# Kernel tuning notes

Measured on AMD Instinct MI355X. Metric: run time of the kernel, lower is better.

Reference implementation:

```python
import jax, jax.numpy as jnp
import numpy as np

B, H, S, D = 4, 16, 2048, 64

def setup_inputs() -> dict:
    key = jax.random.key(0)
    k1, k2, k3 = jax.random.split(key, 3)
    x1 = jax.random.normal(k1, (B, H, S, D), dtype=jnp.float32)
    x2 = jax.random.normal(k2, (B, H, S, D), dtype=jnp.float32)
    x3 = jax.random.normal(k3, (B, H, S, D), dtype=jnp.float32)
    scale = jnp.float32(1.0 / np.sqrt(D))  # 0.125
    return {"x1": x1, "x2": x2, "x3": x3, "scale": scale}

def reference(x1, x2, x3, scale):
    # scores: [B, H, S, S] = Q @ K^T * scale
    scores = jnp.einsum('bhqd,bhkd->bhqk', x1, x2) * scale
    att = jax.nn.softmax(scores, axis=-1)
    # out: [B, H, S, D] = att @ V
    return jnp.einsum('bhqk,bhkd->bhqd', att, x3)
```

## Files before the change

kernel.cpp:

```cpp
#include <hip/hip_runtime.h>
#include <hip/hip_bf16.h>

typedef __attribute__((ext_vector_type(8))) short short8;
typedef __attribute__((ext_vector_type(16))) float f32x16;
typedef __attribute__((ext_vector_type(2))) unsigned uint2v;
typedef unsigned long long ull;

#define S_LEN 2048
#define D_DIM 64
#define QT 256
#define KT 64
#define NT (S_LEN / KT)
#define SMAXC 16.0f
#define SWZ(r) ((((r) & 7) ^ (((r) >> 3) & 7)) << 4)

static __device__ __forceinline__ unsigned cvt_pk(float lo, float hi) {
  unsigned r;
  asm("v_cvt_pk_bf16_f32 %0, %1, %2" : "=v"(r) : "v"(lo), "v"(hi));
  return r;
}

static __device__ __forceinline__ void plswap(unsigned &a, unsigned &b) {
  uint2v r = __builtin_amdgcn_permlane32_swap(a, b, false, false);
  a = r.x; b = r.y;
}

union U8 { unsigned u[4]; short8 s; };

__global__ __attribute__((amdgpu_flat_work_group_size(256, 256),
                          amdgpu_waves_per_eu(2, 2)))
void attn_fwd(const float* __restrict__ Qg, const float* __restrict__ Kg,
              const float* __restrict__ Vg, const float* __restrict__ sp,
              float* __restrict__ Og)
{
  __shared__ __align__(16) char smem[32768];

  const int tid = threadIdx.x;
  const int w   = tid >> 6;
  const int l   = tid & 63;
  const int q32 = l & 31;
  const int hi  = l >> 5;

  const int wg   = blockIdx.x;
  const int xcd  = wg & 7;
  const int slot = wg >> 3;
  const int bh   = xcd * 8 + (slot >> 3);
  const int qb   = (slot & 7) * QT;

  const float* Qh = Qg + (size_t)bh * (S_LEN * D_DIM);
  const float* Kh = Kg + (size_t)bh * (S_LEN * D_DIM);
  const float* Vh = Vg + (size_t)bh * (S_LEN * D_DIM);
  float*       Oh = Og + (size_t)bh * (S_LEN * D_DIM);

  const float qscale = sp[0] * 1.4426950408889634f;

  short8 qfa[4], qfb[4];
#pragma unroll
  for (int qs = 0; qs < 2; ++qs) {
    const float* qrow = Qh + (size_t)(qb + w * 64 + qs * 32 + q32) * D_DIM + hi * 8;
#pragma unroll
    for (int dk = 0; dk < 4; ++dk) {
      float4 f0 = *(const float4*)(qrow + dk * 16);
      float4 f1 = *(const float4*)(qrow + dk * 16 + 4);
      U8 u;
      u.u[0] = cvt_pk(f0.x * qscale, f0.y * qscale);
      u.u[1] = cvt_pk(f0.z * qscale, f0.w * qscale);
      u.u[2] = cvt_pk(f1.x * qscale, f1.y * qscale);
      u.u[3] = cvt_pk(f1.z * qscale, f1.w * qscale);
      if (qs == 0) qfa[dk] = u.s; else qfb[dk] = u.s;
    }
  }

  f32x16 o0a, o1a, o0b, o1b;
#pragma unroll
  for (int r = 0; r < 16; ++r) { o0a[r] = 0.f; o1a[r] = 0.f; o0b[r] = 0.f; o1b[r] = 0.f; }
  float l_a = 0.f, l_b = 0.f;

  const int krow = tid >> 2, kcolf = (tid & 3) * 16;
  const int vdd  = (tid & 15) * 4, vkk = (tid >> 4) * 4;
  const int kd0  = (krow << 7) + ((kcolf * 2) ^ SWZ(krow));
  const int vdo0 = 8192 + ((vdd + 0) << 7) + ((vkk * 2) ^ SWZ(vdd + 0));
  const int vdo1 = 8192 + ((vdd + 1) << 7) + ((vkk * 2) ^ SWZ(vdd + 1));
  const int vdo2 = 8192 + ((vdd + 2) << 7) + ((vkk * 2) ^ SWZ(vdd + 2));
  const int vdo3 = 8192 + ((vdd + 3) << 7) + ((vkk * 2) ^ SWZ(vdd + 3));

  const int swzA = SWZ(q32);
  const int swzB = swzA ^ 64;
  const int kq   = (q32 << 7);

  const float* kptr = Kh + (size_t)krow * D_DIM + kcolf;
  const float* vptr = Vh + (size_t)vkk * D_DIM + vdd;

  {
    float4 a = ((const float4*)kptr)[0], b = ((const float4*)kptr)[1];
    float4 c = ((const float4*)kptr)[2], d = ((const float4*)kptr)[3];
    *(uint4*)(smem + kd0) = make_uint4(cvt_pk(a.x, a.y), cvt_pk(a.z, a.w),
                                       cvt_pk(b.x, b.y), cvt_pk(b.z, b.w));
    *(uint4*)(smem + (kd0 ^ 16)) = make_uint4(cvt_pk(c.x, c.y), cvt_pk(c.z, c.w),
                                              cvt_pk(d.x, d.y), cvt_pk(d.z, d.w));
    float4 r0 = *(const float4*)(vptr);
    float4 r1 = *(const float4*)(vptr + D_DIM);
    float4 r2 = *(const float4*)(vptr + 2 * D_DIM);
    float4 r3 = *(const float4*)(vptr + 3 * D_DIM);
    *(ull*)(smem + vdo0) = ((ull)cvt_pk(r2.x, r3.x) << 32) | cvt_pk(r0.x, r1.x);
    *(ull*)(smem + vdo1) = ((ull)cvt_pk(r2.y, r3.y) << 32) | cvt_pk(r0.y, r1.y);
    *(ull*)(smem + vdo2) = ((ull)cvt_pk(r2.z, r3.z) << 32) | cvt_pk(r0.z, r1.z);
    *(ull*)(smem + vdo3) = ((ull)cvt_pk(r2.w, r3.w) << 32) | cvt_pk(r0.w, r1.w);
  }
  __syncthreads();

  for (int t = 0; t < NT; ++t) {
    const int buf  = (t & 1) * 16384;
    const int bufw = buf ^ 16384;
    const bool more = (t + 1 < NT);

    float4 pa, pb, pc, pd, va, vbq, vc, vdq;
    if (more) {
      const float* ks = kptr + (size_t)(t + 1) * (KT * D_DIM);
      const float* vs = vptr + (size_t)(t + 1) * (KT * D_DIM);
      pa = ((const float4*)ks)[0]; pb = ((const float4*)ks)[1];
      pc = ((const float4*)ks)[2]; pd = ((const float4*)ks)[3];
      va  = *(const float4*)(vs);
      vbq = *(const float4*)(vs + D_DIM);
      vc  = *(const float4*)(vs + 2 * D_DIM);
      vdq = *(const float4*)(vs + 3 * D_DIM);
    }

    const int vb0 = buf + 8192 + kq;
    const int vb1 = vb0 + 4096;

    auto SB = [&](const int sb) {
      const int kbo  = buf + kq + (sb ? 4096 : 0);
      const int swzK = sb ? swzB : swzA;
      f32x16 sta, stb;
#pragma unroll
      for (int r = 0; r < 16; ++r) { sta[r] = -SMAXC; stb[r] = -SMAXC; }
      __builtin_amdgcn_s_setprio(1);
#pragma unroll
      for (int dk = 0; dk < 4; ++dk) {
        short8 ka = *(const short8*)(smem + kbo + ((dk * 32 + hi * 16) ^ swzK));
        sta = __builtin_amdgcn_mfma_f32_32x32x16_bf16(ka, qfa[dk], sta, 0, 0, 0);
        stb = __builtin_amdgcn_mfma_f32_32x32x16_bf16(ka, qfb[dk], stb, 0, 0, 0);
      }
      __builtin_amdgcn_s_setprio(0);

      U8 f0a, f1a, f0b, f1b;
      {
        float s0 = 0.f, s1 = 0.f, s2 = 0.f, s3 = 0.f;
#pragma unroll
        for (int r = 0; r < 16; ++r) {
          sta[r] = __builtin_amdgcn_exp2f(sta[r]);
          if ((r & 3) == 0)      s0 += sta[r];
          else if ((r & 3) == 1) s1 += sta[r];
          else if ((r & 3) == 2) s2 += sta[r];
          else                   s3 += sta[r];
        }
        l_a += (s0 + s1) + (s2 + s3);
        unsigned pk[8];
#pragma unroll
        for (int j = 0; j < 8; ++j) pk[j] = cvt_pk(sta[2 * j], sta[2 * j + 1]);
        plswap(pk[0], pk[2]); plswap(pk[1], pk[3]);
        plswap(pk[4], pk[6]); plswap(pk[5], pk[7]);
        f0a.u[0] = pk[0]; f0a.u[1] = pk[1]; f0a.u[2] = pk[2]; f0a.u[3] = pk[3];
        f1a.u[0] = pk[4]; f1a.u[1] = pk[5]; f1a.u[2] = pk[6]; f1a.u[3] = pk[7];
      }
      {
        float s0 = 0.f, s1 = 0.f, s2 = 0.f, s3 = 0.f;
#pragma unroll
        for (int r = 0; r < 16; ++r) {
          stb[r] = __builtin_amdgcn_exp2f(stb[r]);
          if ((r & 3) == 0)      s0 += stb[r];
          else if ((r & 3) == 1) s1 += stb[r];
          else if ((r & 3) == 2) s2 += stb[r];
          else                   s3 += stb[r];
        }
        l_b += (s0 + s1) + (s2 + s3);
        unsigned pk[8];
#pragma unroll
        for (int j = 0; j < 8; ++j) pk[j] = cvt_pk(stb[2 * j], stb[2 * j + 1]);
        plswap(pk[0], pk[2]); plswap(pk[1], pk[3]);
        plswap(pk[4], pk[6]); plswap(pk[5], pk[7]);
        f0b.u[0] = pk[0]; f0b.u[1] = pk[1]; f0b.u[2] = pk[2]; f0b.u[3] = pk[3];
        f1b.u[0] = pk[4]; f1b.u[1] = pk[5]; f1b.u[2] = pk[6]; f1b.u[3] = pk[7];
      }

      __builtin_amdgcn_s_setprio(1);
      {
        short8 x0 = *(const short8*)(smem + vb0 + ((sb * 64 + 0  + hi * 16) ^ swzA));
        short8 x1 = *(const short8*)(smem + vb0 + ((sb * 64 + 32 + hi * 16) ^ swzA));
        o0a = __builtin_amdgcn_mfma_f32_32x32x16_bf16(x0, f0a.s, o0a, 0, 0, 0);
        o0b = __builtin_amdgcn_mfma_f32_32x32x16_bf16(x0, f0b.s, o0b, 0, 0, 0);
        o0a = __builtin_amdgcn_mfma_f32_32x32x16_bf16(x1, f1a.s, o0a, 0, 0, 0);
        o0b = __builtin_amdgcn_mfma_f32_32x32x16_bf16(x1, f1b.s, o0b, 0, 0, 0);
        short8 y0 = *(const short8*)(smem + vb1 + ((sb * 64 + 0  + hi * 16) ^ swzB));
        short8 y1 = *(const short8*)(smem + vb1 + ((sb * 64 + 32 + hi * 16) ^ swzB));
        o1a = __builtin_amdgcn_mfma_f32_32x32x16_bf16(y0, f0a.s, o1a, 0, 0, 0);
        o1b = __builtin_amdgcn_mfma_f32_32x32x16_bf16(y0, f0b.s, o1b, 0, 0, 0);
        o1a = __builtin_amdgcn_mfma_f32_32x32x16_bf16(y1, f1a.s, o1a, 0, 0, 0);
        o1b = __builtin_amdgcn_mfma_f32_32x32x16_bf16(y1, f1b.s, o1b, 0, 0, 0);
      }
      __builtin_amdgcn_s_setprio(0);
    };

    SB(0);

    if (more) {
      *(uint4*)(smem + bufw + kd0) =
          make_uint4(cvt_pk(pa.x, pa.y), cvt_pk(pa.z, pa.w),
                     cvt_pk(pb.x, pb.y), cvt_pk(pb.z, pb.w));
      *(uint4*)(smem + bufw + (kd0 ^ 16)) =
          make_uint4(cvt_pk(pc.x, pc.y), cvt_pk(pc.z, pc.w),
                     cvt_pk(pd.x, pd.y), cvt_pk(pd.z, pd.w));
    }

    SB(1);

    if (more) {
      *(ull*)(smem + bufw + vdo0) = ((ull)cvt_pk(vc.x, vdq.x) << 32) | cvt_pk(va.x, vbq.x);
      *(ull*)(smem + bufw + vdo1) = ((ull)cvt_pk(vc.y, vdq.y) << 32) | cvt_pk(va.y, vbq.y);
      *(ull*)(smem + bufw + vdo2) = ((ull)cvt_pk(vc.z, vdq.z) << 32) | cvt_pk(va.z, vbq.z);
      *(ull*)(smem + bufw + vdo3) = ((ull)cvt_pk(vc.w, vdq.w) << 32) | cvt_pk(va.w, vbq.w);
    }
    __syncthreads();
  }

  float la_t = l_a + __shfl_xor(l_a, 32, 64);
  float lb_t = l_b + __shfl_xor(l_b, 32, 64);
  float rla = 1.0f / la_t;
  float rlb = 1.0f / lb_t;
  float* Ow = (float*)smem + w * (32 * 36);
#pragma unroll
  for (int qs = 0; qs < 2; ++qs) {
    const float rl = qs ? rlb : rla;
    const int rowbase = qb + w * 64 + qs * 32;
#pragma unroll
    for (int nb = 0; nb < 2; ++nb) {
      __syncthreads();
#pragma unroll
      for (int rr = 0; rr < 4; ++rr) {
        float4 v;
        if (qs == 0) {
          if (nb == 0) { v.x = o0a[rr*4+0]*rl; v.y = o0a[rr*4+1]*rl; v.z = o0a[rr*4+2]*rl; v.w = o0a[rr*4+3]*rl; }
          else         { v.x = o1a[rr*4+0]*rl; v.y = o1a[rr*4+1]*rl; v.z = o1a[rr*4+2]*rl; v.w = o1a[rr*4+3]*rl; }
        } else {
          if (nb == 0) { v.x = o0b[rr*4+0]*rl; v.y = o0b[rr*4+1]*rl; v.z = o0b[rr*4+2]*rl; v.w = o0b[rr*4+3]*rl; }
          else         { v.x = o1b[rr*4+0]*rl; v.y = o1b[rr*4+1]*rl; v.z = o1b[rr*4+2]*rl; v.w = o1b[rr*4+3]*rl; }
        }
        *(float4*)&Ow[q32 * 36 + rr * 8 + hi * 4] = v;
      }
      __syncthreads();
#pragma unroll
      for (int i = 0; i < 4; ++i) {
        int e = i * 256 + l * 4;
        int row = e >> 5, col = e & 31;
        float4 v = *(const float4*)&Ow[row * 36 + col];
        *(float4*)(Oh + (size_t)(rowbase + row) * D_DIM + nb * 32 + col) = v;
      }
    }
  }
}

extern "C" void kernel_launch(void* const* d_in, const int* in_sizes, int n_in,
                              void* d_out, int out_size, void* d_ws, size_t ws_size,
                              hipStream_t stream) {
  (void)in_sizes; (void)n_in; (void)d_ws; (void)ws_size; (void)out_size;
  const float* Q  = (const float*)d_in[0];
  const float* K  = (const float*)d_in[1];
  const float* V  = (const float*)d_in[2];
  const float* sp = (const float*)d_in[3];
  float* O = (float*)d_out;
  dim3 grid((S_LEN / QT) * 64);
  attn_fwd<<<grid, 256, 0, stream>>>(Q, K, V, sp, O);
}
```

Baseline: 89.54 us.

## Software-pipeline QK MFMAs ahead of softmax with triple-buffered LDS and staggered starts

Moves to a software-pipelined schedule. The QK^T MFMA for the next sub-block is issued before the exp/pack and PV of the current one, so matrix work can overlap the VALU softmax. LDS grows to three 16KB buffers so the next tile can be written, and then read after one barrier, while the current tile's V half is still in use. Half of the workgroups also sleep briefly at launch to stagger phases. The costs are more registers for the extra score accumulators, more LDS per block, and an added startup delay for some blocks.

Result: slower. 108.9 us (+21.6%).

```diff
diff --git a/kernel.cpp b/kernel.cpp
--- a/kernel.cpp
+++ b/kernel.cpp
@@ -12,6 +12,7 @@
 #define KT 64
 #define NT (S_LEN / KT)
 #define SMAXC 16.0f
+#define BUFSZ 16384
 #define SWZ(r) ((((r) & 7) ^ (((r) >> 3) & 7)) << 4)
 
 static __device__ __forceinline__ unsigned cvt_pk(float lo, float hi) {
@@ -33,7 +34,7 @@
               const float* __restrict__ Vg, const float* __restrict__ sp,
               float* __restrict__ Og)
 {
-  __shared__ __align__(16) char smem[32768];
+  __shared__ __align__(16) char smem[49152];
 
   const int tid = threadIdx.x;
   const int w   = tid >> 6;
@@ -46,6 +47,10 @@
   const int slot = wg >> 3;
   const int bh   = xcd * 8 + (slot >> 3);
   const int qb   = (slot & 7) * QT;
+
+  if ((slot ^ (slot >> 5)) & 1) {
+    __builtin_amdgcn_s_sleep(48);
+  }
 
   const float* Qh = Qg + (size_t)bh * (S_LEN * D_DIM);
   const float* Kh = Kg + (size_t)bh * (S_LEN * D_DIM);
@@ -109,9 +114,81 @@
   }
   __syncthreads();
 
+  f32x16 sta_S0, stb_S0, sta_S1, stb_S1;
+#pragma unroll
+  for (int r = 0; r < 16; ++r) { sta_S0[r] = -SMAXC; stb_S0[r] = -SMAXC; }
+  __builtin_amdgcn_s_setprio(1);
+#pragma unroll
+  for (int dk = 0; dk < 4; ++dk) {
+    short8 ka = *(const short8*)(smem + kq + ((dk * 32 + hi * 16) ^ swzA));
+    sta_S0 = __builtin_amdgcn_mfma_f32_32x32x16_bf16(ka, qfa[dk], sta_S0, 0, 0, 0);
+    stb_S0 = __builtin_amdgcn_mfma_f32_32x32x16_bf16(ka, qfb[dk], stb_S0, 0, 0, 0);
+  }
+  __builtin_amdgcn_s_setprio(0);
+
+  int cur = 0, nxt = BUFSZ, nx2 = 2 * BUFSZ;
+
+  auto SMPACK = [&](f32x16& sta, f32x16& stb, U8& f0a, U8& f1a, U8& f0b, U8& f1b) {
+    {
+      float s0 = 0.f, s1 = 0.f, s2 = 0.f, s3 = 0.f;
+#pragma unroll
+      for (int r = 0; r < 16; ++r) {
+        sta[r] = __builtin_amdgcn_exp2f(sta[r]);
+        if ((r & 3) == 0)      s0 += sta[r];
+        else if ((r & 3) == 1) s1 += sta[r];
+        else if ((r & 3) == 2) s2 += sta[r];
+        else                   s3 += sta[r];
+      }
+      l_a += (s0 + s1) + (s2 + s3);
+      unsigned pk[8];
+#pragma unroll
+      for (int j = 0; j < 8; ++j) pk[j] = cvt_pk(sta[2 * j], sta[2 * j + 1]);
+      plswap(pk[0], pk[2]); plswap(pk[1], pk[3]);
+      plswap(pk[4], pk[6]); plswap(pk[5], pk[7]);
+      f0a.u[0] = pk[0]; f0a.u[1] = pk[1]; f0a.u[2] = pk[2]; f0a.u[3] = pk[3];
+      f1a.u[0] = pk[4]; f1a.u[1] = pk[5]; f1a.u[2] = pk[6]; f1a.u[3] = pk[7];
+    }
+    {
+      float s0 = 0.f, s1 = 0.f, s2 = 0.f, s3 = 0.f;
+#pragma unroll
+      for (int r = 0; r < 16; ++r) {
+        stb[r] = __builtin_amdgcn_exp2f(stb[r]);
+        if ((r & 3) == 0)      s0 += stb[r];
+        else if ((r & 3) == 1) s1 += stb[r];
+        else if ((r & 3) == 2) s2 += stb[r];
+        else                   s3 += stb[r];
+      }
+      l_b += (s0 + s1) + (s2 + s3);
+      unsigned pk[8];
+#pragma unroll
+      for (int j = 0; j < 8; ++j) pk[j] = cvt_pk(stb[2 * j], stb[2 * j + 1]);
+      plswap(pk[0], pk[2]); plswap(pk[1], pk[3]);
+      plswap(pk[4], pk[6]); plswap(pk[5], pk[7]);
+      f0b.u[0] = pk[0]; f0b.u[1] = pk[1]; f0b.u[2] = pk[2]; f0b.u[3] = pk[3];
+      f1b.u[0] = pk[4]; f1b.u[1] = pk[5]; f1b.u[2] = pk[6]; f1b.u[3] = pk[7];
+    }
+  };
+
+  auto PV = [&](int bufo, int vo, U8& f0a, U8& f1a, U8& f0b, U8& f1b) {
+    const int vb0 = bufo + 8192 + kq;
+    const int vb1 = vb0 + 4096;
+    __builtin_amdgcn_s_setprio(1);
+    short8 x0 = *(const short8*)(smem + vb0 + ((vo + 0  + hi * 16) ^ swzA));
+    short8 x1 = *(const short8*)(smem + vb0 + ((vo + 32 + hi * 16) ^ swzA));
+    o0a = __builtin_amdgcn_mfma_f32_32x32x16_bf16(x0, f0a.s, o0a, 0, 0, 0);
+    o0b = __builtin_amdgcn_mfma_f32_32x32x16_bf16(x0, f0b.s, o0b, 0, 0, 0);
+    o0a = __builtin_amdgcn_mfma_f32_32x32x16_bf16(x1, f1a.s, o0a, 0, 0, 0);
+    o0b = __builtin_amdgcn_mfma_f32_32x32x16_bf16(x1, f1b.s, o0b, 0, 0, 0);
+    short8 y0 = *(const short8*)(smem + vb1 + ((vo + 0  + hi * 16) ^ swzB));
+    short8 y1 = *(const short8*)(smem + vb1 + ((vo + 32 + hi * 16) ^ swzB));
+    o1a = __builtin_amdgcn_mfma_f32_32x32x16_bf16(y0, f0a.s, o1a, 0, 0, 0);
+    o1b = __builtin_amdgcn_mfma_f32_32x32x16_bf16(y0, f0b.s, o1b, 0, 0, 0);
+    o1a = __builtin_amdgcn_mfma_f32_32x32x16_bf16(y1, f1a.s, o1a, 0, 0, 0);
+    o1b = __builtin_amdgcn_mfma_f32_32x32x16_bf16(y1, f1b.s, o1b, 0, 0, 0);
+    __builtin_amdgcn_s_setprio(0);
+  };
+
   for (int t = 0; t < NT; ++t) {
-    const int buf  = (t & 1) * 16384;
-    const int bufw = buf ^ 16384;
     const bool more = (t + 1 < NT);
 
     float4 pa, pb, pc, pd, va, vbq, vc, vdq;
@@ -126,102 +203,53 @@
       vdq = *(const float4*)(vs + 3 * D_DIM);
     }
 
-    const int vb0 = buf + 8192 + kq;
-    const int vb1 = vb0 + 4096;
-
-    auto SB = [&](const int sb) {
-      const int kbo  = buf + kq + (sb ? 4096 : 0);
-      const int swzK = sb ? swzB : swzA;
-      f32x16 sta, stb;
-#pragma unroll
-      for (int r = 0; r < 16; ++r) { sta[r] = -SMAXC; stb[r] = -SMAXC; }
-      __builtin_amdgcn_s_setprio(1);
-#pragma unroll
-      for (int dk = 0; dk < 4; ++dk) {
-        short8 ka = *(const short8*)(smem + kbo + ((dk * 32 + hi * 16) ^ swzK));
-        sta = __builtin_amdgcn_mfma_f32_32x32x16_bf16(ka, qfa[dk], sta, 0, 0, 0);
-        stb = __builtin_amdgcn_mfma_f32_32x32x16_bf16(ka, qfb[dk], stb, 0, 0, 0);
-      }
-      __builtin_amdgcn_s_setprio(0);
-
-      U8 f0a, f1a, f0b, f1b;
-      {
-        float s0 = 0.f, s1 = 0.f, s2 = 0.f, s3 = 0.f;
-#pragma unroll
-        for (int r = 0; r < 16; ++r) {
-          sta[r] = __builtin_amdgcn_exp2f(sta[r]);
-          if ((r & 3) == 0)      s0 += sta[r];
-          else if ((r & 3) == 1) s1 += sta[r];
-          else if ((r & 3) == 2) s2 += sta[r];
-          else                   s3 += sta[r];
-        }
-        l_a += (s0 + s1) + (s2 + s3);
-        unsigned pk[8];
-#pragma unroll
-        for (int j = 0; j < 8; ++j) pk[j] = cvt_pk(sta[2 * j], sta[2 * j + 1]);
-        plswap(pk[0], pk[2]); plswap(pk[1], pk[3]);
-        plswap(pk[4], pk[6]); plswap(pk[5], pk[7]);
-        f0a.u[0] = pk[0]; f0a.u[1] = pk[1]; f0a.u[2] = pk[2]; f0a.u[3] = pk[3];
-        f1a.u[0] = pk[4]; f1a.u[1] = pk[5]; f1a.u[2] = pk[6]; f1a.u[3] = pk[7];
-      }
-      {
-        float s0 = 0.f, s1 = 0.f, s2 = 0.f, s3 = 0.f;
-#pragma unroll
-        for (int r = 0; r < 16; ++r) {
-          stb[r] = __builtin_amdgcn_exp2f(stb[r]);
-          if ((r & 3) == 0)      s0 += stb[r];
-          else if ((r & 3) == 1) s1 += stb[r];
-          else if ((r & 3) == 2) s2 += stb[r];
-          else                   s3 += stb[r];
-        }
-        l_b += (s0 + s1) + (s2 + s3);
-        unsigned pk[8];
-#pragma unroll
-        for (int j = 0; j < 8; ++j) pk[j] = cvt_pk(stb[2 * j], stb[2 * j + 1]);
-        plswap(pk[0], pk[2]); plswap(pk[1], pk[3]);
-        plswap(pk[4], pk[6]); plswap(pk[5], pk[7]);
-        f0b.u[0] = pk[0]; f0b.u[1] = pk[1]; f0b.u[2] = pk[2]; f0b.u[3] = pk[3];
-        f1b.u[0] = pk[4]; f1b.u[1] = pk[5]; f1b.u[2] = pk[6]; f1b.u[3] = pk[7];
-      }
-
-      __builtin_amdgcn_s_setprio(1);
-      {
-        short8 x0 = *(const short8*)(smem + vb0 + ((sb * 64 + 0  + hi * 16) ^ swzA));
-        short8 x1 = *(const short8*)(smem + vb0 + ((sb * 64 + 32 + hi * 16) ^ swzA));
-        o0a = __builtin_amdgcn_mfma_f32_32x32x16_bf16(x0, f0a.s, o0a, 0, 0, 0);
-        o0b = __builtin_amdgcn_mfma_f32_32x32x16_bf16(x0, f0b.s, o0b, 0, 0, 0);
-        o0a = __builtin_amdgcn_mfma_f32_32x32x16_bf16(x1, f1a.s, o0a, 0, 0, 0);
-        o0b = __builtin_amdgcn_mfma_f32_32x32x16_bf16(x1, f1b.s, o0b, 0, 0, 0);
-        short8 y0 = *(const short8*)(smem + vb1 + ((sb * 64 + 0  + hi * 16) ^ swzB));
-        short8 y1 = *(const short8*)(smem + vb1 + ((sb * 64 + 32 + hi * 16) ^ swzB));
-        o1a = __builtin_amdgcn_mfma_f32_32x32x16_bf16(y0, f0a.s, o1a, 0, 0, 0);
-        o1b = __builtin_amdgcn_mfma_f32_32x32x16_bf16(y0, f0b.s, o1b, 0, 0, 0);
-        o1a = __builtin_amdgcn_mfma_f32_32x32x16_bf16(y1, f1a.s, o1a, 0, 0, 0);
-        o1b = __builtin_amdgcn_mfma_f32_32x32x16_bf16(y1, f1b.s, o1b, 0, 0, 0);
-      }
-      __builtin_amdgcn_s_setprio(0);
-    };
-
-    SB(0);
+#pragma unroll
+    for (int r = 0; r < 16; ++r) { sta_S1[r] = -SMAXC; stb_S1[r] = -SMAXC; }
+    __builtin_amdgcn_s_setprio(1);
+#pragma unroll
+    for (int dk = 0; dk < 4; ++dk) {
+      short8 ka = *(const short8*)(smem + cur + kq + 4096 + ((dk * 32 + hi * 16) ^ swzB));
+      sta_S1 = __builtin_amdgcn_mfma_f32_32x32x16_bf16(ka, qfa[dk], sta_S1, 0, 0, 0);
+      stb_S1 = __builtin_amdgcn_mfma_f32_32x32x16_bf16(ka, qfb[dk], stb_S1, 0, 0, 0);
+    }
+    __builtin_amdgcn_s_setprio(0);
+
+    U8 f0a, f1a, f0b, f1b;
+    SMPACK(sta_S0, stb_S0, f0a, f1a, f0b, f1b);
+    PV(cur, 0, f0a, f1a, f0b, f1b);
 
     if (more) {
-      *(uint4*)(smem + bufw + kd0) =
+      *(uint4*)(smem + nxt + kd0) =
           make_uint4(cvt_pk(pa.x, pa.y), cvt_pk(pa.z, pa.w),
                      cvt_pk(pb.x, pb.y), cvt_pk(pb.z, pb.w));
-      *(uint4*)(smem + bufw + (kd0 ^ 16)) =
+      *(uint4*)(smem + nxt + (kd0 ^ 16)) =
           make_uint4(cvt_pk(pc.x, pc.y), cvt_pk(pc.z, pc.w),
                      cvt_pk(pd.x, pd.y), cvt_pk(pd.z, pd.w));
-    }
-
-    SB(1);
+      *(ull*)(smem + nxt + vdo0) = ((ull)cvt_pk(vc.x, vdq.x) << 32) | cvt_pk(va.x, vbq.x);
+      *(ull*)(smem + nxt + vdo1) = ((ull)cvt_pk(vc.y, vdq.y) << 32) | cvt_pk(va.y, vbq.y);
+      *(ull*)(smem + nxt + vdo2) = ((ull)cvt_pk(vc.z, vdq.z) << 32) | cvt_pk(va.z, vbq.z);
+      *(ull*)(smem + nxt + vdo3) = ((ull)cvt_pk(vc.w, vdq.w) << 32) | cvt_pk(va.w, vbq.w);
+    }
+
+    __syncthreads();
 
     if (more) {
-      *(ull*)(smem + bufw + vdo0) = ((ull)cvt_pk(vc.x, vdq.x) << 32) | cvt_pk(va.x, vbq.x);
-      *(ull*)(smem + bufw + vdo1) = ((ull)cvt_pk(vc.y, vdq.y) << 32) | cvt_pk(va.y, vbq.y);
-      *(ull*)(smem + bufw + vdo2) = ((ull)cvt_pk(vc.z, vdq.z) << 32) | cvt_pk(va.z, vbq.z);
-      *(ull*)(smem + bufw + vdo3) = ((ull)cvt_pk(vc.w, vdq.w) << 32) | cvt_pk(va.w, vbq.w);
-    }
-    __syncthreads();
+#pragma unroll
+      for (int r = 0; r < 16; ++r) { sta_S0[r] = -SMAXC; stb_S0[r] = -SMAXC; }
+      __builtin_amdgcn_s_setprio(1);
+#pragma unroll
+      for (int dk = 0; dk < 4; ++dk) {
+        short8 ka = *(const short8*)(smem + nxt + kq + ((dk * 32 + hi * 16) ^ swzA));
+        sta_S0 = __builtin_amdgcn_mfma_f32_32x32x16_bf16(ka, qfa[dk], sta_S0, 0, 0, 0);
+        stb_S0 = __builtin_amdgcn_mfma_f32_32x32x16_bf16(ka, qfb[dk], stb_S0, 0, 0, 0);
+      }
+      __builtin_amdgcn_s_setprio(0);
+    }
+
+    SMPACK(sta_S1, stb_S1, f0a, f1a, f0b, f1b);
+    PV(cur, 64, f0a, f1a, f0b, f1b);
+
+    int tmp = cur; cur = nxt; nxt = nx2; nx2 = tmp;
   }
 
   float la_t = l_a + __shfl_xor(l_a, 32, 64);
```
